# Optimization experiments

Measured on AMD Instinct MI355X. Metric: run time of the kernel, lower is better.

The kernel has to match this reference:

```python
import jax, jax.numpy as jnp
import numpy as np

GH = 256       # GRU hidden size
VOCAB = 1000
MAX_EP = 150
NPREV = NCURR = NNEXT = 64


def _gru_scan(emb, h0, wih, whh, bih, bhh):
    # torch nn.GRU single-layer math, scanned over the token axis
    H = h0.shape[0]
    def step(h, x_t):
        gi = wih @ x_t + bih            # [3H]
        gh = whh @ h + bhh              # [3H]
        r = jax.nn.sigmoid(gi[:H] + gh[:H])
        z = jax.nn.sigmoid(gi[H:2 * H] + gh[H:2 * H])
        n = jnp.tanh(gi[2 * H:] + r * gh[2 * H:])
        hn = (1.0 - z) * n + z * h
        return hn, hn
    _, hs = jax.lax.scan(step, h0, emb)
    return hs                            # [L, H]


def _conv(x, w, b, s):
    y = jax.lax.conv_general_dilated(x, w, (s, s), 'VALID',
                                     dimension_numbers=('NCHW', 'OIHW', 'NCHW'))
    return y + b[None, :, None, None]


def setup_inputs():
    key = jax.random.key(0)
    ks = jax.random.split(key, 48)
    f32 = jnp.float32
    def W(i, shape, s=0.05):
        return (jax.random.normal(ks[i], shape) * s).astype(f32)
    inp = dict(
        x=jax.random.normal(ks[0], (1, 3, 124, 124), f32),
        hx=jax.random.normal(ks[1], (1, 256), f32),
        cx=jax.random.normal(ks[2], (1, 256), f32),
        conv1_w=W(3, (128, 3, 8, 8)), conv1_b=jnp.zeros((128,), f32),
        conv2_w=W(4, (64, 128, 4, 4)), conv2_b=jnp.zeros((64,), f32),
        conv3_w=W(5, (64, 64, 4, 4)), conv3_b=jnp.zeros((64,), f32),
        emb_w=W(6, (VOCAB, 32), 1.0),
        gru_f_wih=W(7, (3 * GH, 32)), gru_f_whh=W(8, (3 * GH, GH)),
        gru_f_bih=jnp.zeros((3 * GH,), f32), gru_f_bhh=jnp.zeros((3 * GH,), f32),
        gru_b_wih=W(9, (3 * GH, 32)), gru_b_whh=W(10, (3 * GH, GH)),
        gru_b_bih=jnp.zeros((3 * GH,), f32), gru_b_bhh=jnp.zeros((3 * GH,), f32),
        time_emb_w=W(11, (MAX_EP + 1, 32), 1.0),
        temp_emb_w=W(12, (2, 32), 1.0),
        img_emb_w=W(13, (256, 64 * 6 * 6)), img_emb_b=jnp.zeros((256,), f32),
        attn_key_w=W(14, (256, 256 * 3)), attn_key_b=jnp.zeros((256,), f32),
        bilinear_A=W(15, (1, 256, 544)), bilinear_b=jnp.zeros((1,), f32),
        reduce_w=W(16, (128, 544)), reduce_b=jnp.zeros((128,), f32),
        gate_w=W(17, (64, 640)), gate_b=jnp.zeros((64,), f32),
        lin_w=W(18, (256, 64 * 6 * 6)), lin_b=jnp.zeros((256,), f32),
        lstm_wih=W(19, (1024, 256)), lstm_whh=W(20, (1024, 256)),
        lstm_bih=jnp.zeros((1024,), f32), lstm_bhh=jnp.zeros((1024,), f32),
        critic_w=W(21, (1, 288)), critic_b=jnp.zeros((1,), f32),
        actor_w=W(22, (4, 288)), actor_b=jnp.zeros((4,), f32),
        prev_inst=jax.random.randint(ks[23], (1, NPREV), 0, VOCAB),
        curr_inst=jax.random.randint(ks[24], (1, NCURR), 0, VOCAB),
        next_inst=jax.random.randint(ks[25], (1, NNEXT), 0, VOCAB),
        tx=jax.random.randint(ks[26], (1,), 0, MAX_EP + 1),
    )
    return inp


def reference(x, hx, cx, conv1_w, conv1_b, conv2_w, conv2_b, conv3_w, conv3_b,
              emb_w, gru_f_wih, gru_f_whh, gru_f_bih, gru_f_bhh,
              gru_b_wih, gru_b_whh, gru_b_bih, gru_b_bhh,
              time_emb_w, temp_emb_w, img_emb_w, img_emb_b,
              attn_key_w, attn_key_b, bilinear_A, bilinear_b,
              reduce_w, reduce_b, gate_w, gate_b, lin_w, lin_b,
              lstm_wih, lstm_whh, lstm_bih, lstm_bhh,
              critic_w, critic_b, actor_w, actor_b,
              prev_inst, curr_inst, next_inst, tx):
    np_, nc, nn_ = prev_inst.shape[1], curr_inst.shape[1], next_inst.shape[1]
    all_inst = jnp.concatenate([prev_inst, curr_inst, next_inst], axis=1)[0]  # [L]
    L = all_inst.shape[0]

    # CNN encoder
    h = jax.nn.relu(_conv(x, conv1_w, conv1_b, 4))
    h = jax.nn.relu(_conv(h, conv2_w, conv2_b, 2))
    x_img = jax.nn.relu(_conv(h, conv3_w, conv3_b, 2))       # [1,64,6,6]

    # token-looped GRUs -> single lax.scan each (note: original runs gru_b
    # over the SAME forward order then reverses the hidden list; replicated)
    emb = emb_w[all_inst]                                    # [L,32]
    h0 = jnp.zeros((GH,), emb.dtype)
    hs_f = _gru_scan(emb, h0, gru_f_wih, gru_f_whh, gru_f_bih, gru_f_bhh)
    hs_b = _gru_scan(emb, h0, gru_b_wih, gru_b_whh, gru_b_bih, gru_b_bhh)[::-1]
    curr_instr_rep = jnp.concatenate([hs_f[np_ + nc - 1], hs_b[np_]])[None]  # [1,512]
    ir_f = jnp.concatenate([hs_f[:np_], hs_f[L - nn_:]], axis=0)             # [M,256]
    ir_b = jnp.concatenate([hs_b[:np_], hs_b[L - nn_:]], axis=0)
    temp_tok = jnp.concatenate([jnp.zeros((np_,), jnp.int32), jnp.ones((nn_,), jnp.int32)])
    instr_rep = jnp.concatenate([ir_f, ir_b, temp_emb_w[temp_tok]], axis=1)  # [M,544]

    # bilinear attention over prev/next token states
    image_emb = x_img.reshape(1, -1) @ img_emb_w.T + img_emb_b               # [1,256]
    attn_key = jnp.concatenate([curr_instr_rep, image_emb], 1) @ attn_key_w.T + attn_key_b
    scores = jnp.einsum('k,okv,mv->mo', attn_key[0], bilinear_A, instr_rep) + bilinear_b  # [M,1]
    w = jax.nn.softmax(scores, axis=0)
    instr_sum = (instr_rep * w).sum(0, keepdims=True)                        # [1,544]

    # gating of image features
    gating = instr_sum @ reduce_w.T + reduce_b                               # [1,128]
    gate_key = jax.nn.sigmoid(jnp.concatenate([curr_instr_rep, gating], 1) @ gate_w.T + gate_b)  # [1,64]
    xg = (x_img * gate_key[:, :, None, None]).reshape(1, -1)
    z = jax.nn.relu(xg @ lin_w.T + lin_b)                                    # [1,256]

    # LSTMCell (torch gate order i,f,g,o)
    gates = z @ lstm_wih.T + lstm_bih + hx @ lstm_whh.T + lstm_bhh           # [1,1024]
    i, f, g, o = jnp.split(gates, 4, axis=1)
    cx2 = jax.nn.sigmoid(f) * cx + jax.nn.sigmoid(i) * jnp.tanh(g)
    hx2 = jax.nn.sigmoid(o) * jnp.tanh(cx2)

    feat = jnp.concatenate([hx2, time_emb_w[tx].reshape(-1, 32)], axis=1)    # [1,288]
    critic = feat @ critic_w.T + critic_b                                    # [1,1]
    actor = feat @ actor_w.T + actor_b                                       # [1,4]
    return critic, actor, hx2, cx2
```

## Files before the change

kernel.cpp:

```cpp
#include <hip/hip_runtime.h>
#include <hip/hip_bf16.h>

typedef int int4v __attribute__((ext_vector_type(4)));

__device__ __forceinline__ float bf2f(unsigned short u) {
    unsigned int v = ((unsigned int)u) << 16;
    return __builtin_bit_cast(float, v);
}
__device__ __forceinline__ float sigm(float x) { return 1.0f / (1.0f + expf(-x)); }
__device__ __forceinline__ float san(float v) {
    return (v == v && fabsf(v) < 1e20f) ? v : 12345.0f;
}
__device__ __forceinline__ void wrout(void* out, int i, float v, int f32out) {
    if (f32out) ((float*)out)[i] = v;
    else ((__hip_bfloat16*)out)[i] = __float2bfloat16(v);
}
__device__ __forceinline__ float fexp2(float x) {
#if __has_builtin(__builtin_amdgcn_exp2f)
    return __builtin_amdgcn_exp2f(x);
#else
    return exp2f(x);
#endif
}
__device__ __forceinline__ float frcp(float x) {
#if __has_builtin(__builtin_amdgcn_rcpf)
    return __builtin_amdgcn_rcpf(x);
#else
    return 1.0f / x;
#endif
}
__device__ __forceinline__ float fsigm(float x) {
    return frcp(1.0f + fexp2(x * -1.44269504f));
}
__device__ __forceinline__ float ftanh(float x) {
    float t = fexp2(x * 2.88539008f);
    return 1.0f - 2.0f * frcp(t + 1.0f);
}
__device__ __forceinline__ float wave_red(float acc) {
#pragma unroll
    for (int off = 32; off >= 1; off >>= 1) acc += __shfl_down(acc, off);
    return acc;
}
__device__ __forceinline__ int sel4(int4v v, int rg) {
    int a = (rg & 1) ? v.y : v.x;
    int b = (rg & 1) ? v.w : v.z;
    return (rg & 2) ? b : a;
}

struct CanonArgs {
    const void* ptr[40];
    int start[41];
    int size[40];
};

__global__ void k_flag1000(void* out) {
    if (threadIdx.x == 0) ((unsigned int*)out)[0] = 0x447A0000u;
}

__global__ void k_detect_tokens(const void* x, int nx,
                                const int* __restrict__ prev, const int* __restrict__ curr,
                                const int* __restrict__ nxt, const int* __restrict__ tx,
                                float* __restrict__ flags, int* __restrict__ toks) {
    __shared__ float sm[256];
    __shared__ int sInt64;
    int tid = threadIdx.x;
    const unsigned short* xs = (const unsigned short*)x;
    float mx = 0.0f;
    for (int i = tid; i < nx; i += 256) {
        float f = bf2f(xs[i]);
        float a = (f == f) ? fabsf(f) : 1e30f;
        mx = fmaxf(mx, a);
    }
    sm[tid] = mx;
    __syncthreads();
    for (int s = 128; s >= 1; s >>= 1) {
        if (tid < s) sm[tid] = fmaxf(sm[tid], sm[tid + s]);
        __syncthreads();
    }
    if (tid == 0) {
        flags[0] = (sm[0] > 100.0f) ? 1.0f : 0.0f;
        int anyOdd = 0;
        for (int k = 0; k < 32; ++k) anyOdd |= curr[2 * k + 1];
        int i64 = (anyOdd == 0) ? 1 : 0;
        flags[1] = (float)i64;
        sInt64 = i64;
    }
    __syncthreads();
    int stride = sInt64 ? 2 : 1;
    if (tid < 192) {
        const int* src = (tid < 64) ? prev : ((tid < 128) ? curr : nxt);
        int v = src[(tid & 63) * stride];
        toks[tid] = min(max(v, 0), 999);
    }
    if (tid == 0) toks[192] = min(max(tx[0], 0), 150);
}

__global__ void k_convert(CanonArgs a, const float* __restrict__ flags,
                          float* __restrict__ C) {
    int base = blockIdx.x << 10;
    int t = 0;
    while (t < 39 && base >= a.start[t + 1]) ++t;
    int local = base - a.start[t] + (threadIdx.x << 2);
    int sz = a.size[t];
    float4 v = make_float4(0.0f, 0.0f, 0.0f, 0.0f);
    int f32in = (flags[0] != 0.0f);
    if (local + 3 < sz) {
        if (f32in) {
            v = *(const float4*)((const float*)a.ptr[t] + local);
        } else {
            uint2 u = *(const uint2*)((const unsigned short*)a.ptr[t] + local);
            v.x = bf2f((unsigned short)(u.x & 0xffff));
            v.y = bf2f((unsigned short)(u.x >> 16));
            v.z = bf2f((unsigned short)(u.y & 0xffff));
            v.w = bf2f((unsigned short)(u.y >> 16));
        }
    } else if (local < sz) {
        float tmp[4] = {0.0f, 0.0f, 0.0f, 0.0f};
        for (int q = 0; q < 4 && local + q < sz; ++q) {
            if (f32in) tmp[q] = ((const float*)a.ptr[t])[local + q];
            else tmp[q] = bf2f(((const unsigned short*)a.ptr[t])[local + q]);
        }
        v = make_float4(tmp[0], tmp[1], tmp[2], tmp[3]);
    }
    *(float4*)(C + base + (threadIdx.x << 2)) = v;
}

__global__ void k_conv1(const float* __restrict__ x, const float* __restrict__ w,
                        const float* __restrict__ b, float* __restrict__ out) {
    int idx = blockIdx.x * 256 + threadIdx.x;
    int oc = idx / 900;
    int rem = idx - oc * 900;
    int oh = rem / 30;
    int ow = rem - oh * 30;
    float acc = b[oc];
    for (int ic = 0; ic < 3; ++ic) {
        int xb = ic * 15376 + (oh * 4) * 124 + ow * 4;
        int wb = oc * 192 + ic * 64;
#pragma unroll
        for (int kh = 0; kh < 8; ++kh) {
            const float2* xr = (const float2*)(x + xb + kh * 124);
            const float2* wr = (const float2*)(w + wb + kh * 8);
#pragma unroll
            for (int p = 0; p < 4; ++p) {
                float2 xv = xr[p];
                float2 wv = wr[p];
                acc += xv.x * wv.x + xv.y * wv.y;
            }
        }
    }
    out[idx] = fmaxf(acc, 0.0f);
}

__global__ void k_conv2(const float* __restrict__ in, const float* __restrict__ w,
                        const float* __restrict__ b, float* __restrict__ out) {
    int wid = (blockIdx.x * 256 + threadIdx.x) >> 6;
    int lane = threadIdx.x & 63;
    int oc = wid / 196;
    int rem = wid - oc * 196;
    int oh = rem / 14, ow = rem - oh * 14;
    float acc = 0.0f;
#pragma unroll 8
    for (int i = 0; i < 32; ++i) {
        int e = lane + (i << 6);
        int ic = e >> 4, k = e & 15, kh = k >> 2, kw = k & 3;
        acc += in[ic * 900 + (oh * 2 + kh) * 30 + ow * 2 + kw] * w[oc * 2048 + e];
    }
    acc = wave_red(acc);
    if (lane == 0) out[wid] = fmaxf(acc + b[oc], 0.0f);
}

__global__ void k_conv3(const float* __restrict__ in, const float* __restrict__ w,
                        const float* __restrict__ b, float* __restrict__ out) {
    int wid = (blockIdx.x * 256 + threadIdx.x) >> 6;
    int lane = threadIdx.x & 63;
    int oc = wid / 36;
    int rem = wid - oc * 36;
    int oh = rem / 6, ow = rem - oh * 6;
    float acc = 0.0f;
#pragma unroll
    for (int i = 0; i < 16; ++i) {
        int e = lane + (i << 6);
        int ic = e >> 4, k = e & 15, kh = k >> 2, kw = k & 3;
        acc += in[ic * 196 + (oh * 2 + kh) * 14 + ow * 2 + kw] * w[oc * 1024 + e];
    }
    acc = wave_red(acc);
    if (lane == 0) out[wid] = fmaxf(acc + b[oc], 0.0f);
}

__global__ void k_imgemb(const float* __restrict__ ximg, const float* __restrict__ w,
                         const float* __restrict__ b, float* __restrict__ out) {
    int j = blockIdx.x;
    int t = threadIdx.x;
    const float* wr = w + j * 2304;
    float acc = 0.0f;
    for (int k = t; k < 2304; k += 64) acc += wr[k] * ximg[k];
    acc = wave_red(acc);
    if (t == 0) out[j] = acc + b[j];
}

__global__ void k_gi(const int* __restrict__ toks, const float* __restrict__ emb,
                     const float* __restrict__ wih_f, const float* __restrict__ bih_f,
                     const float* __restrict__ bhh_f,
                     const float* __restrict__ wih_b, const float* __restrict__ bih_b,
                     const float* __restrict__ bhh_b,
                     float* __restrict__ gi) {
    int t = blockIdx.y;
    int gru = blockIdx.z;
    int j = blockIdx.x * 256 + threadIdx.x;
    __shared__ float e[32];
    int tok = toks[t];
    if (threadIdx.x < 32) e[threadIdx.x] = emb[tok * 32 + threadIdx.x];
    __syncthreads();
    const float* wih = gru ? wih_b : wih_f;
    const float* bih = gru ? bih_b : bih_f;
    const float* bhh = gru ? bhh_b : bhh_f;
    const float2* wr = (const float2*)(wih + j * 32);
    float acc = bih[j] + ((j < 512) ? bhh[j] : 0.0f);
#pragma unroll
    for (int k = 0; k < 16; ++k) {
        float2 wv = wr[k];
        acc += wv.x * e[2 * k] + wv.y * e[2 * k + 1];
    }
    gi[(gru * 192 + t) * 768 + j] = acc;
}

__global__ __launch_bounds__(512, 1) void k_gru(
    const float* __restrict__ whh_f, const float* __restrict__ bhh_f,
    const float* __restrict__ whh_b, const float* __restrict__ bhh_b,
    const float* __restrict__ gi, float* __restrict__ hs) {
    __shared__ unsigned int hq[2][64];
    __shared__ float sc[768];

    int gru = blockIdx.x;
    const float* whh = gru ? whh_b : whh_f;
    const float* bhh = gru ? bhh_b : bhh_f;
    const float* gib = gi + gru * 192 * 768;
    float* hso = hs + gru * 192 * 256;

    int t = threadIdx.x;
    int l = t & 63;
    int w = t >> 6;
    int lg = l >> 4;
    int lr = l & 15;
    int e_sel = (l >> 2) & 1;
    int rg = l & 3;
    int j = 32 * w + 16 * e_sel + 4 * lg + rg;

    int4v A[3][2][4];
#pragma unroll
    for (int s3 = 0; s3 < 3; ++s3) {
#pragma unroll
        for (int e = 0; e < 2; ++e) {
            int r = s3 * 256 + 32 * w + 16 * e + lr;
            const float* rowp = whh + r * 256;
            float4 tmp[16];
            float mx = 0.0f;
#pragma unroll
            for (int q = 0; q < 4; ++q) {
#pragma unroll
                for (int f = 0; f < 4; ++f) {
                    float4 v = *(const float4*)(rowp + 64 * q + 16 * lg + 4 * f);
                    tmp[q * 4 + f] = v;
                    mx = fmaxf(mx, fmaxf(fmaxf(fabsf(v.x), fabsf(v.y)),
                                         fmaxf(fabsf(v.z), fabsf(v.w))));
                }
            }
            mx = fmaxf(mx, __shfl_xor(mx, 16));
            mx = fmaxf(mx, __shfl_xor(mx, 32));
            float scale = 127.0f / fmaxf(mx, 1e-20f);
            if (lg == 0) sc[r] = mx * (1.0f / (127.0f * 127.0f));
#pragma unroll
            for (int q = 0; q < 4; ++q) {
                int dw[4];
#pragma unroll
                for (int f = 0; f < 4; ++f) {
                    float4 v = tmp[q * 4 + f];
                    int p0 = (int)rintf(v.x * scale) & 0xff;
                    int p1 = (int)rintf(v.y * scale) & 0xff;
                    int p2 = (int)rintf(v.z * scale) & 0xff;
                    int p3 = (int)rintf(v.w * scale);
                    dw[f] = p0 | (p1 << 8) | (p2 << 16) | (p3 << 24);
                }
                A[s3][e][q] = (int4v){dw[0], dw[1], dw[2], dw[3]};
            }
        }
    }
    if (t < 128) ((unsigned int*)hq)[t] = 0u;
    __syncthreads();

    float invR = sc[j];
    float invZ = sc[256 + j];
    float invN = sc[512 + j];
    float bhhn = bhh[512 + j];
    int wr8 = ((l & 8) == 0);

    float hprev = 0.0f;
    float cr0 = gib[j],       cz0 = gib[256 + j],  cn0 = gib[512 + j];
    float cr1 = gib[768 + j], cz1 = gib[1024 + j], cn1 = gib[1280 + j];

    int4v zero4 = (int4v){0, 0, 0, 0};

    auto step = [&](const unsigned int* hbuf, unsigned int* hnxt, int S,
                    float gr, float gz, float gn) {
        const char* hb = (const char*)hbuf;
        int4v B0 = *(const int4v*)(hb + 16 * lg);
        int4v B1 = *(const int4v*)(hb + 64 + 16 * lg);
        int4v B2 = *(const int4v*)(hb + 128 + 16 * lg);
        int4v B3 = *(const int4v*)(hb + 192 + 16 * lg);

        int4v C00, C01, C10, C11, C20, C21;
        asm volatile(
            "v_mfma_i32_16x16x64_i8 %0, %7,  %31, %6\n\t"
            "v_mfma_i32_16x16x64_i8 %1, %11, %31, %6\n\t"
            "v_mfma_i32_16x16x64_i8 %2, %15, %31, %6\n\t"
            "v_mfma_i32_16x16x64_i8 %3, %19, %31, %6\n\t"
            "v_mfma_i32_16x16x64_i8 %4, %23, %31, %6\n\t"
            "v_mfma_i32_16x16x64_i8 %5, %27, %31, %6\n\t"
            "v_mfma_i32_16x16x64_i8 %0, %8,  %32, %0\n\t"
            "v_mfma_i32_16x16x64_i8 %1, %12, %32, %1\n\t"
            "v_mfma_i32_16x16x64_i8 %2, %16, %32, %2\n\t"
            "v_mfma_i32_16x16x64_i8 %3, %20, %32, %3\n\t"
            "v_mfma_i32_16x16x64_i8 %4, %24, %32, %4\n\t"
            "v_mfma_i32_16x16x64_i8 %5, %28, %32, %5\n\t"
            "v_mfma_i32_16x16x64_i8 %0, %9,  %33, %0\n\t"
            "v_mfma_i32_16x16x64_i8 %1, %13, %33, %1\n\t"
            "v_mfma_i32_16x16x64_i8 %2, %17, %33, %2\n\t"
            "v_mfma_i32_16x16x64_i8 %3, %21, %33, %3\n\t"
            "v_mfma_i32_16x16x64_i8 %4, %25, %33, %4\n\t"
            "v_mfma_i32_16x16x64_i8 %5, %29, %33, %5\n\t"
            "v_mfma_i32_16x16x64_i8 %0, %10, %34, %0\n\t"
            "v_mfma_i32_16x16x64_i8 %1, %14, %34, %1\n\t"
            "v_mfma_i32_16x16x64_i8 %2, %18, %34, %2\n\t"
            "v_mfma_i32_16x16x64_i8 %3, %22, %34, %3\n\t"
            "v_mfma_i32_16x16x64_i8 %4, %26, %34, %4\n\t"
            "v_mfma_i32_16x16x64_i8 %5, %30, %34, %5\n\t"
            "s_nop 7\n\t"
            "s_nop 7"
            : "=&v"(C00), "=&v"(C01), "=&v"(C10),
              "=&v"(C11), "=&v"(C20), "=&v"(C21)
            : "v"(zero4),
              "v"(A[0][0][0]), "v"(A[0][0][1]), "v"(A[0][0][2]), "v"(A[0][0][3]),
              "v"(A[0][1][0]), "v"(A[0][1][1]), "v"(A[0][1][2]), "v"(A[0][1][3]),
              "v"(A[1][0][0]), "v"(A[1][0][1]), "v"(A[1][0][2]), "v"(A[1][0][3]),
              "v"(A[1][1][0]), "v"(A[1][1][1]), "v"(A[1][1][2]), "v"(A[1][1][3]),
              "v"(A[2][0][0]), "v"(A[2][0][1]), "v"(A[2][0][2]), "v"(A[2][0][3]),
              "v"(A[2][1][0]), "v"(A[2][1][1]), "v"(A[2][1][2]), "v"(A[2][1][3]),
              "v"(B0), "v"(B1), "v"(B2), "v"(B3));
        __builtin_amdgcn_sched_barrier(0);

        int ri = sel4(e_sel ? C01 : C00, rg);
        int zi = sel4(e_sel ? C11 : C10, rg);
        int ni = sel4(e_sel ? C21 : C20, rg);
        float ar = (float)ri * invR;
        float az = (float)zi * invZ;
        float an = (float)ni * invN;
        float r = fsigm(gr + ar);
        float z = fsigm(gz + az);
        float n = ftanh(gn + r * (an + bhhn));
        hprev = z * (hprev - n) + n;

        int qv = (int)rintf(hprev * 127.0f);
        if (wr8) {
            hso[S * 256 + j] = hprev;
            ((char*)hnxt)[j] = (char)qv;
        }
        asm volatile("s_waitcnt lgkmcnt(0)" ::: "memory");
        __builtin_amdgcn_s_barrier();
    };

    for (int i = 0; i < 96; ++i) {
        int s0 = 2 * i;
        float nr0 = 0.0f, nz0 = 0.0f, nn0 = 0.0f;
        if (s0 + 2 < 192) {
            const float* gp = gib + (s0 + 2) * 768 + j;
            nr0 = gp[0]; nz0 = gp[256]; nn0 = gp[512];
        }
        step(&hq[0][0], &hq[1][0], s0, cr0, cz0, cn0);

        int s1 = s0 + 1;
        float nr1 = 0.0f, nz1 = 0.0f, nn1 = 0.0f;
        if (s1 + 2 < 192) {
            const float* gp = gib + (s1 + 2) * 768 + j;
            nr1 = gp[0]; nz1 = gp[256]; nn1 = gp[512];
        }
        step(&hq[1][0], &hq[0][0], s1, cr1, cz1, cn1);

        cr0 = nr0; cz0 = nz0; cn0 = nn0;
        cr1 = nr1; cz1 = nz1; cn1 = nn1;
    }
}

__device__ __forceinline__ float ir_val(int m, int v, const float* hsf, const float* hsb,
                                        const float* temp_emb) {
    if (v < 256) { int r = (m < 64) ? m : 64 + m; return hsf[r * 256 + v]; }
    if (v < 512) { int r = (m < 64) ? 191 - m : 127 - m; return hsb[r * 256 + v - 256]; }
    return temp_emb[(m >= 64) * 32 + (v - 512)];
}

__global__ void k_attnkey(const float* __restrict__ hs, const float* __restrict__ imgemb,
                          const float* __restrict__ w, const float* __restrict__ b,
                          float* __restrict__ ak) {
    int j = blockIdx.x;
    int t = threadIdx.x;
    const float* hsf127 = hs + 127 * 256;
    const float* hsb127 = hs + 192 * 256 + 127 * 256;
    const float* wr = w + j * 768;
    float acc = 0.0f;
    for (int k = t; k < 768; k += 64) {
        float v = (k < 256) ? hsf127[k] : ((k < 512) ? hsb127[k - 256] : imgemb[k - 512]);
        acc += wr[k] * v;
    }
    acc = wave_red(acc);
    if (t == 0) ak[j] = acc + b[j];
}

__global__ void k_bilin(const float* __restrict__ A, const float* __restrict__ ak,
                        float* __restrict__ tmp) {
    int v = blockIdx.x;
    int t = threadIdx.x;
    float acc = 0.0f;
#pragma unroll
    for (int k = t; k < 256; k += 64) acc += A[k * 544 + v] * ak[k];
    acc = wave_red(acc);
    if (t == 0) tmp[v] = acc;
}

__global__ __launch_bounds__(1024) void k_attnmid(
    const float* __restrict__ hs, const float* __restrict__ temp_emb_w,
    const float* __restrict__ tmpv, const float* __restrict__ bb,
    const float* __restrict__ reduce_w, const float* __restrict__ reduce_b,
    const float* __restrict__ gate_w, const float* __restrict__ gate_b,
    float* __restrict__ gk) {
    const int tid = threadIdx.x;
    const float* hsf = hs;
    const float* hsb = hs + 192 * 256;
    __shared__ float stmp[544], ssc[128], ssum[544], sred[1024], sgating[128], scr[512];

    if (tid < 256) {
        scr[tid] = hsf[127 * 256 + tid];
        scr[256 + tid] = hsb[127 * 256 + tid];
    }
    if (tid < 544) stmp[tid] = tmpv[tid];
    __syncthreads();

    {
        int m = tid >> 3, q = tid & 7;
        float acc = 0.0f;
        for (int v = q * 68; v < q * 68 + 68; ++v) acc += stmp[v] * ir_val(m, v, hsf, hsb, temp_emb_w);
        sred[tid] = acc;
    }
    __syncthreads();
    if (tid < 128) {
        float acc = bb[0];
        for (int q = 0; q < 8; ++q) acc += sred[tid * 8 + q];
        ssc[tid] = acc;
        sred[tid] = acc;
    }
    __syncthreads();
#pragma unroll
    for (int s2 = 64; s2 >= 1; s2 >>= 1) {
        if (tid < s2) sred[tid] = fmaxf(sred[tid], sred[tid + s2]);
        __syncthreads();
    }
    float mx = sred[0];
    __syncthreads();
    if (tid < 128) {
        float e = expf(ssc[tid] - mx);
        ssc[tid] = e;
        sred[tid] = e;
    }
    __syncthreads();
#pragma unroll
    for (int s2 = 64; s2 >= 1; s2 >>= 1) {
        if (tid < s2) sred[tid] += sred[tid + s2];
        __syncthreads();
    }
    float inv = 1.0f / sred[0];
    __syncthreads();
    if (tid < 128) ssc[tid] *= inv;
    __syncthreads();

    if (tid < 544) {
        float acc = 0.0f;
        for (int m = 0; m < 128; ++m) acc += ssc[m] * ir_val(m, tid, hsf, hsb, temp_emb_w);
        ssum[tid] = acc;
    }
    __syncthreads();

    {
        int j = tid >> 3, q = tid & 7;
        const float2* wr = (const float2*)(reduce_w + j * 544 + q * 68);
        float acc = 0.0f;
        for (int k = 0; k < 34; ++k) {
            float2 wv = wr[k];
            acc += wv.x * ssum[q * 68 + 2 * k] + wv.y * ssum[q * 68 + 2 * k + 1];
        }
        sred[tid] = acc;
    }
    __syncthreads();
    if (tid < 128) {
        float acc = reduce_b[tid];
        for (int q = 0; q < 8; ++q) acc += sred[tid * 8 + q];
        sgating[tid] = acc;
    }
    __syncthreads();

    {
        int j = tid >> 4, q = tid & 15;
        const float2* wr = (const float2*)(gate_w + j * 640 + q * 40);
        float acc = 0.0f;
        for (int k = 0; k < 20; ++k) {
            float2 wv = wr[k];
            int v0 = q * 40 + 2 * k;
            float a0 = (v0 < 512) ? scr[v0] : sgating[v0 - 512];
            float a1 = (v0 + 1 < 512) ? scr[v0 + 1] : sgating[v0 + 1 - 512];
            acc += wv.x * a0 + wv.y * a1;
        }
        sred[tid] = acc;
    }
    __syncthreads();
    if (tid < 64) {
        float acc = gate_b[tid];
        for (int q = 0; q < 16; ++q) acc += sred[tid * 16 + q];
        gk[tid] = sigm(acc);
    }
}

__global__ void k_lin(const float* __restrict__ ximg, const float* __restrict__ gk,
                      const float* __restrict__ w, const float* __restrict__ b,
                      float* __restrict__ z) {
    int j = blockIdx.x;
    int t = threadIdx.x;
    __shared__ float sgk[64];
    if (t < 64) sgk[t] = gk[t];
    __syncthreads();
    const float* wr = w + j * 2304;
    float acc = 0.0f;
    for (int k = t; k < 2304; k += 64) acc += wr[k] * ximg[k] * sgk[k / 36];
    acc = wave_red(acc);
    if (t == 0) z[j] = fmaxf(acc + b[j], 0.0f);
}

__global__ void k_lstm(const float* __restrict__ z, const float* __restrict__ hx,
                       const float* __restrict__ wih, const float* __restrict__ whh,
                       const float* __restrict__ bih, const float* __restrict__ bhh,
                       float* __restrict__ sg) {
    int j = blockIdx.x;
    int t = threadIdx.x;
    const float* wi = wih + j * 256;
    const float* wh = whh + j * 256;
    float acc = 0.0f;
#pragma unroll
    for (int k = t; k < 256; k += 64) acc += wi[k] * z[k] + wh[k] * hx[k];
    acc = wave_red(acc);
    if (t == 0) sg[j] = acc + bih[j] + bhh[j];
}

__global__ __launch_bounds__(1024) void k_final(
    const float* __restrict__ sgg, const float* __restrict__ cx,
    const float* __restrict__ time_emb_w, const int* __restrict__ toks,
    const float* __restrict__ critic_w, const float* __restrict__ critic_b,
    const float* __restrict__ actor_w, const float* __restrict__ actor_b,
    const float* __restrict__ flags, void* __restrict__ out) {
    const int tid = threadIdx.x;
    __shared__ float sfeat[288], shx2[256], scx2[256], stmp[544], sred[1024];

    if (tid < 256) {
        float ii = sgg[tid], ff = sgg[256 + tid], gg = sgg[512 + tid], oo = sgg[768 + tid];
        float c2 = sigm(ff) * cx[tid] + sigm(ii) * tanhf(gg);
        float h2 = sigm(oo) * tanhf(c2);
        scx2[tid] = c2;
        shx2[tid] = h2;
        sfeat[tid] = h2;
    }
    if (tid < 32) sfeat[256 + tid] = time_emb_w[toks[192] * 32 + tid];
    __syncthreads();

    if (tid < 512) stmp[tid] = (tid < 288) ? critic_w[tid] * sfeat[tid] : 0.0f;
    {
        int a = tid >> 8, k = tid & 255;
        float pa = actor_w[a * 288 + k] * sfeat[k];
        if (k < 32) pa += actor_w[a * 288 + 256 + k] * sfeat[256 + k];
        sred[tid] = pa;
    }
    __syncthreads();
#pragma unroll
    for (int s2 = 256; s2 >= 1; s2 >>= 1) {
        if (tid < s2) stmp[tid] += stmp[tid + s2];
        int k = tid & 255;
        if (s2 <= 128 && k < s2) sred[tid] += sred[tid + s2];
        __syncthreads();
    }

    int f32out = (flags[0] != 0.0f) ? 1 : 0;
    if (tid == 0) wrout(out, 0, san(stmp[0] + critic_b[0]), f32out);
    if (tid < 4) wrout(out, 1 + tid, san(sred[tid * 256] + actor_b[tid]), f32out);
    if (tid < 256) {
        wrout(out, 5 + tid, san(shx2[tid]), f32out);
        wrout(out, 261 + tid, san(scx2[tid]), f32out);
    }
}

extern "C" void kernel_launch(void* const* d_in, const int* in_sizes, int n_in,
                              void* d_out, int out_size, void* d_ws, size_t ws_size,
                              hipStream_t stream) {
    if (n_in != 44) return;

    CanonArgs ca;
    int acc = 0;
    for (int i = 0; i < 40; ++i) {
        ca.ptr[i] = d_in[i];
        ca.start[i] = acc;
        ca.size[i] = in_sizes[i];
        acc += (in_sizes[i] + 1023) & ~1023;
    }
    ca.start[40] = acc;
    const int T = acc;

    float* ws     = (float*)d_ws;
    float* flags  = ws;
    int*   toks   = (int*)(ws + 64);
    float* imgemb = ws + 320;
    float* C      = ws + 640;
    float* gi     = C + T;
    float* hs     = gi + 294912;
    float* aux    = hs + 98304;
    float* ak     = aux;
    float* tmpv   = aux + 256;
    float* gk     = aux + 928;
    float* zv     = aux + 992;
    float* sg     = aux + 1248;
    float* h1     = gi;
    float* h2     = h1 + 115200;
    float* ximg   = h2 + 12544;

    size_t need = (size_t)(640 + T + 294912 + 98304 + 2272) * 4;
    if (ws_size < need) {
        k_flag1000<<<1, 64, 0, stream>>>(d_out);
        return;
    }

    const int* prev = (const int*)d_in[40];
    const int* curr = (const int*)d_in[41];
    const int* nxt  = (const int*)d_in[42];
    const int* tx   = (const int*)d_in[43];

    k_detect_tokens<<<1, 256, 0, stream>>>(d_in[0], in_sizes[0], prev, curr, nxt, tx,
                                           flags, toks);
    k_convert<<<T >> 10, 256, 0, stream>>>(ca, flags, C);

#define CP(i) (C + ca.start[i])
    k_gi<<<dim3(3, 192, 2), 256, 0, stream>>>(toks, CP(9),
                                              CP(10), CP(12), CP(13),
                                              CP(14), CP(16), CP(17), gi);
    k_gru<<<2, 512, 0, stream>>>(CP(11), CP(13), CP(15), CP(17), gi, hs);
    k_conv1<<<450, 256, 0, stream>>>(CP(0), CP(3), CP(4), h1);
    k_conv2<<<3136, 256, 0, stream>>>(h1, CP(5), CP(6), h2);
    k_conv3<<<576, 256, 0, stream>>>(h2, CP(7), CP(8), ximg);
    k_imgemb<<<256, 64, 0, stream>>>(ximg, CP(20), CP(21), imgemb);
    k_attnkey<<<256, 64, 0, stream>>>(hs, imgemb, CP(22), CP(23), ak);
    k_bilin<<<544, 64, 0, stream>>>(CP(24), ak, tmpv);
    k_attnmid<<<1, 1024, 0, stream>>>(hs, CP(19), tmpv, CP(25),
                                      CP(26), CP(27), CP(28), CP(29), gk);
    k_lin<<<256, 64, 0, stream>>>(ximg, gk, CP(30), CP(31), zv);
    k_lstm<<<1024, 64, 0, stream>>>(zv, CP(1), CP(32), CP(33), CP(34), CP(35), sg);
    k_final<<<1, 1024, 0, stream>>>(sg, CP(2), CP(18), toks,
                                    CP(36), CP(37), CP(38), CP(39), flags, d_out);
#undef CP
}
```

Before: 482.8 us.

## Overlap GRU recurrence with conv stack in one kernel and fuse tail kernels

Merges the two-block GRU scan and the conv1/conv2/conv3/image-embedding chain into one persistent kernel. Blocks 0-1 run the GRU while 128 other blocks run the convolutions, separated by a grid-wide atomic barrier, so the image path runs in the GRU's shadow. The attention, gating, linear, LSTM and output kernels are folded into a single 1024-thread tail kernel to remove launch overheads. The cost is a spin barrier that relies on all blocks being co-resident, and a single block doing the tail matvecs with less parallelism.

Result: slower. 736.9 us (+52.6%).

```diff
diff --git a/kernel.cpp b/kernel.cpp
--- a/kernel.cpp
+++ b/kernel.cpp
@@ -2,6 +2,8 @@
 #include <hip/hip_bf16.h>
 
 typedef int int4v __attribute__((ext_vector_type(4)));
+
+#define CBLK 128
 
 __device__ __forceinline__ float bf2f(unsigned short u) {
     unsigned int v = ((unsigned int)u) << 16;
@@ -45,6 +47,18 @@
     int a = (rg & 1) ? v.y : v.x;
     int b = (rg & 1) ? v.w : v.z;
     return (rg & 2) ? b : a;
+}
+
+__device__ __forceinline__ void gbar(unsigned int* bar, unsigned int target) {
+    __syncthreads();
+    if (threadIdx.x == 0) {
+        __threadfence();
+        atomicAdd(bar, 1u);
+        while (__hip_atomic_load(bar, __ATOMIC_RELAXED, __HIP_MEMORY_SCOPE_AGENT) < target)
+            __builtin_amdgcn_s_sleep(2);
+        __threadfence();
+    }
+    __syncthreads();
 }
 
 struct CanonArgs {
@@ -125,79 +139,6 @@
     *(float4*)(C + base + (threadIdx.x << 2)) = v;
 }
 
-__global__ void k_conv1(const float* __restrict__ x, const float* __restrict__ w,
-                        const float* __restrict__ b, float* __restrict__ out) {
-    int idx = blockIdx.x * 256 + threadIdx.x;
-    int oc = idx / 900;
-    int rem = idx - oc * 900;
-    int oh = rem / 30;
-    int ow = rem - oh * 30;
-    float acc = b[oc];
-    for (int ic = 0; ic < 3; ++ic) {
-        int xb = ic * 15376 + (oh * 4) * 124 + ow * 4;
-        int wb = oc * 192 + ic * 64;
-#pragma unroll
-        for (int kh = 0; kh < 8; ++kh) {
-            const float2* xr = (const float2*)(x + xb + kh * 124);
-            const float2* wr = (const float2*)(w + wb + kh * 8);
-#pragma unroll
-            for (int p = 0; p < 4; ++p) {
-                float2 xv = xr[p];
-                float2 wv = wr[p];
-                acc += xv.x * wv.x + xv.y * wv.y;
-            }
-        }
-    }
-    out[idx] = fmaxf(acc, 0.0f);
-}
-
-__global__ void k_conv2(const float* __restrict__ in, const float* __restrict__ w,
-                        const float* __restrict__ b, float* __restrict__ out) {
-    int wid = (blockIdx.x * 256 + threadIdx.x) >> 6;
-    int lane = threadIdx.x & 63;
-    int oc = wid / 196;
-    int rem = wid - oc * 196;
-    int oh = rem / 14, ow = rem - oh * 14;
-    float acc = 0.0f;
-#pragma unroll 8
-    for (int i = 0; i < 32; ++i) {
-        int e = lane + (i << 6);
-        int ic = e >> 4, k = e & 15, kh = k >> 2, kw = k & 3;
-        acc += in[ic * 900 + (oh * 2 + kh) * 30 + ow * 2 + kw] * w[oc * 2048 + e];
-    }
-    acc = wave_red(acc);
-    if (lane == 0) out[wid] = fmaxf(acc + b[oc], 0.0f);
-}
-
-__global__ void k_conv3(const float* __restrict__ in, const float* __restrict__ w,
-                        const float* __restrict__ b, float* __restrict__ out) {
-    int wid = (blockIdx.x * 256 + threadIdx.x) >> 6;
-    int lane = threadIdx.x & 63;
-    int oc = wid / 36;
-    int rem = wid - oc * 36;
-    int oh = rem / 6, ow = rem - oh * 6;
-    float acc = 0.0f;
-#pragma unroll
-    for (int i = 0; i < 16; ++i) {
-        int e = lane + (i << 6);
-        int ic = e >> 4, k = e & 15, kh = k >> 2, kw = k & 3;
-        acc += in[ic * 196 + (oh * 2 + kh) * 14 + ow * 2 + kw] * w[oc * 1024 + e];
-    }
-    acc = wave_red(acc);
-    if (lane == 0) out[wid] = fmaxf(acc + b[oc], 0.0f);
-}
-
-__global__ void k_imgemb(const float* __restrict__ ximg, const float* __restrict__ w,
-                         const float* __restrict__ b, float* __restrict__ out) {
-    int j = blockIdx.x;
-    int t = threadIdx.x;
-    const float* wr = w + j * 2304;
-    float acc = 0.0f;
-    for (int k = t; k < 2304; k += 64) acc += wr[k] * ximg[k];
-    acc = wave_red(acc);
-    if (t == 0) out[j] = acc + b[j];
-}
-
 __global__ void k_gi(const int* __restrict__ toks, const float* __restrict__ emb,
                      const float* __restrict__ wih_f, const float* __restrict__ bih_f,
                      const float* __restrict__ bhh_f,
@@ -224,169 +165,247 @@
     gi[(gru * 192 + t) * 768 + j] = acc;
 }
 
-__global__ __launch_bounds__(512, 1) void k_gru(
-    const float* __restrict__ whh_f, const float* __restrict__ bhh_f,
-    const float* __restrict__ whh_b, const float* __restrict__ bhh_b,
-    const float* __restrict__ gi, float* __restrict__ hs) {
+struct BigArgs {
+    const float *whh_f, *bhh_f, *whh_b, *bhh_b, *gi;
+    float* hs;
+    const float *x, *c1w, *c1b, *c2w, *c2b, *c3w, *c3b, *iew, *ieb;
+    float *h1, *xh2, *ximg, *imgemb;
+    unsigned int* bars;
+};
+
+__global__ __launch_bounds__(512, 1) void k_big(BigArgs a) {
     __shared__ unsigned int hq[2][64];
     __shared__ float sc[768];
-
-    int gru = blockIdx.x;
-    const float* whh = gru ? whh_b : whh_f;
-    const float* bhh = gru ? bhh_b : bhh_f;
-    const float* gib = gi + gru * 192 * 768;
-    float* hso = hs + gru * 192 * 256;
-
-    int t = threadIdx.x;
-    int l = t & 63;
-    int w = t >> 6;
-    int lg = l >> 4;
-    int lr = l & 15;
-    int e_sel = (l >> 2) & 1;
-    int rg = l & 3;
-    int j = 32 * w + 16 * e_sel + 4 * lg + rg;
-
-    int4v A[3][2][4];
-#pragma unroll
-    for (int s3 = 0; s3 < 3; ++s3) {
-#pragma unroll
-        for (int e = 0; e < 2; ++e) {
-            int r = s3 * 256 + 32 * w + 16 * e + lr;
-            const float* rowp = whh + r * 256;
-            float4 tmp[16];
-            float mx = 0.0f;
-#pragma unroll
-            for (int q = 0; q < 4; ++q) {
-#pragma unroll
-                for (int f = 0; f < 4; ++f) {
-                    float4 v = *(const float4*)(rowp + 64 * q + 16 * lg + 4 * f);
-                    tmp[q * 4 + f] = v;
-                    mx = fmaxf(mx, fmaxf(fmaxf(fabsf(v.x), fabsf(v.y)),
-                                         fmaxf(fabsf(v.z), fabsf(v.w))));
+    const int B = blockIdx.x;
+    const int tid = threadIdx.x;
+
+    if (B < 2) {
+        const float* whh = B ? a.whh_b : a.whh_f;
+        const float* bhh = B ? a.bhh_b : a.bhh_f;
+        const float* gib = a.gi + B * 192 * 768;
+        float* hso = a.hs + B * 192 * 256;
+
+        int t = tid;
+        int l = t & 63;
+        int w = t >> 6;
+        int lg = l >> 4;
+        int lr = l & 15;
+        int e_sel = (l >> 2) & 1;
+        int rg = l & 3;
+        int j = 32 * w + 16 * e_sel + 4 * lg + rg;
+
+        int4v A[3][2][4];
+#pragma unroll
+        for (int s3 = 0; s3 < 3; ++s3) {
+#pragma unroll
+            for (int e = 0; e < 2; ++e) {
+                int r = s3 * 256 + 32 * w + 16 * e + lr;
+                const float* rowp = whh + r * 256;
+                float4 tmp[16];
+                float mx = 0.0f;
+#pragma unroll
+                for (int q = 0; q < 4; ++q) {
+#pragma unroll
+                    for (int f = 0; f < 4; ++f) {
+                        float4 v = *(const float4*)(rowp + 64 * q + 16 * lg + 4 * f);
+                        tmp[q * 4 + f] = v;
+                        mx = fmaxf(mx, fmaxf(fmaxf(fabsf(v.x), fabsf(v.y)),
+                                             fmaxf(fabsf(v.z), fabsf(v.w))));
+                    }
+                }
+                mx = fmaxf(mx, __shfl_xor(mx, 16));
+                mx = fmaxf(mx, __shfl_xor(mx, 32));
+                float scale = 127.0f / fmaxf(mx, 1e-20f);
+                if (lg == 0) sc[r] = mx * (1.0f / (127.0f * 127.0f));
+#pragma unroll
+                for (int q = 0; q < 4; ++q) {
+                    int dw[4];
+#pragma unroll
+                    for (int f = 0; f < 4; ++f) {
+                        float4 v = tmp[q * 4 + f];
+                        int p0 = (int)rintf(v.x * scale) & 0xff;
+                        int p1 = (int)rintf(v.y * scale) & 0xff;
+                        int p2 = (int)rintf(v.z * scale) & 0xff;
+                        int p3 = (int)rintf(v.w * scale);
+                        dw[f] = p0 | (p1 << 8) | (p2 << 16) | (p3 << 24);
+                    }
+                    A[s3][e][q] = (int4v){dw[0], dw[1], dw[2], dw[3]};
                 }
             }
-            mx = fmaxf(mx, __shfl_xor(mx, 16));
-            mx = fmaxf(mx, __shfl_xor(mx, 32));
-            float scale = 127.0f / fmaxf(mx, 1e-20f);
-            if (lg == 0) sc[r] = mx * (1.0f / (127.0f * 127.0f));
-#pragma unroll
-            for (int q = 0; q < 4; ++q) {
-                int dw[4];
-#pragma unroll
-                for (int f = 0; f < 4; ++f) {
-                    float4 v = tmp[q * 4 + f];
-                    int p0 = (int)rintf(v.x * scale) & 0xff;
-                    int p1 = (int)rintf(v.y * scale) & 0xff;
-                    int p2 = (int)rintf(v.z * scale) & 0xff;
-                    int p3 = (int)rintf(v.w * scale);
-                    dw[f] = p0 | (p1 << 8) | (p2 << 16) | (p3 << 24);
+        }
+        if (t < 128) ((unsigned int*)hq)[t] = 0u;
+        __syncthreads();
+
+        float invR = sc[j];
+        float invZ = sc[256 + j];
+        float invN = sc[512 + j];
+        float bhhn = bhh[512 + j];
+        int wr8 = ((l & 8) == 0);
+
+        float hprev = 0.0f;
+        float cr0 = gib[j],       cz0 = gib[256 + j],  cn0 = gib[512 + j];
+        float cr1 = gib[768 + j], cz1 = gib[1024 + j], cn1 = gib[1280 + j];
+
+        int4v zero4 = (int4v){0, 0, 0, 0};
+
+        auto step = [&](const unsigned int* hbuf, unsigned int* hnxt, int S,
+                        float gr, float gz, float gn) {
+            const char* hb = (const char*)hbuf;
+            int4v B0 = *(const int4v*)(hb + 16 * lg);
+            int4v B1 = *(const int4v*)(hb + 64 + 16 * lg);
+            int4v B2 = *(const int4v*)(hb + 128 + 16 * lg);
+            int4v B3 = *(const int4v*)(hb + 192 + 16 * lg);
+
+            int4v C00, C01, C10, C11, C20, C21;
+            asm volatile(
+                "v_mfma_i32_16x16x64_i8 %0, %7,  %31, %6\n\t"
+                "v_mfma_i32_16x16x64_i8 %1, %11, %31, %6\n\t"
+                "v_mfma_i32_16x16x64_i8 %2, %15, %31, %6\n\t"
+                "v_mfma_i32_16x16x64_i8 %3, %19, %31, %6\n\t"
+                "v_mfma_i32_16x16x64_i8 %4, %23, %31, %6\n\t"
+                "v_mfma_i32_16x16x64_i8 %5, %27, %31, %6\n\t"
+                "v_mfma_i32_16x16x64_i8 %0, %8,  %32, %0\n\t"
+                "v_mfma_i32_16x16x64_i8 %1, %12, %32, %1\n\t"
+                "v_mfma_i32_16x16x64_i8 %2, %16, %32, %2\n\t"
+                "v_mfma_i32_16x16x64_i8 %3, %20, %32, %3\n\t"
+                "v_mfma_i32_16x16x64_i8 %4, %24, %32, %4\n\t"
+                "v_mfma_i32_16x16x64_i8 %5, %28, %32, %5\n\t"
+                "v_mfma_i32_16x16x64_i8 %0, %9,  %33, %0\n\t"
+                "v_mfma_i32_16x16x64_i8 %1, %13, %33, %1\n\t"
+                "v_mfma_i32_16x16x64_i8 %2, %17, %33, %2\n\t"
+                "v_mfma_i32_16x16x64_i8 %3, %21, %33, %3\n\t"
+                "v_mfma_i32_16x16x64_i8 %4, %25, %33, %4\n\t"
+                "v_mfma_i32_16x16x64_i8 %5, %29, %33, %5\n\t"
+                "v_mfma_i32_16x16x64_i8 %0, %10, %34, %0\n\t"
+                "v_mfma_i32_16x16x64_i8 %1, %14, %34, %1\n\t"
+                "v_mfma_i32_16x16x64_i8 %2, %18, %34, %2\n\t"
+                "v_mfma_i32_16x16x64_i8 %3, %22, %34, %3\n\t"
+                "v_mfma_i32_16x16x64_i8 %4, %26, %34, %4\n\t"
+                "v_mfma_i32_16x16x64_i8 %5, %30, %34, %5\n\t"
+                "s_nop 7\n\t"
+                "s_nop 7"
+                : "=&v"(C00), "=&v"(C01), "=&v"(C10),
+                  "=&v"(C11), "=&v"(C20), "=&v"(C21)
+                : "v"(zero4),
+                  "v"(A[0][0][0]), "v"(A[0][0][1]), "v"(A[0][0][2]), "v"(A[0][0][3]),
+                  "v"(A[0][1][0]), "v"(A[0][1][1]), "v"(A[0][1][2]), "v"(A[0][1][3]),
+                  "v"(A[1][0][0]), "v"(A[1][0][1]), "v"(A[1][0][2]), "v"(A[1][0][3]),
+                  "v"(A[1][1][0]), "v"(A[1][1][1]), "v"(A[1][1][2]), "v"(A[1][1][3]),
+                  "v"(A[2][0][0]), "v"(A[2][0][1]), "v"(A[2][0][2]), "v"(A[2][0][3]),
+                  "v"(A[2][1][0]), "v"(A[2][1][1]), "v"(A[2][1][2]), "v"(A[2][1][3]),
+                  "v"(B0), "v"(B1), "v"(B2), "v"(B3));
+            __builtin_amdgcn_sched_barrier(0);
+
+            int ri = sel4(e_sel ? C01 : C00, rg);
+            int zi = sel4(e_sel ? C11 : C10, rg);
+            int ni = sel4(e_sel ? C21 : C20, rg);
+            float ar = (float)ri * invR;
+            float az = (float)zi * invZ;
+            float an = (float)ni * invN;
+            float r = fsigm(gr + ar);
+            float z = fsigm(gz + az);
+            float n = ftanh(gn + r * (an + bhhn));
+            hprev = z * (hprev - n) + n;
+
+            int qv = (int)rintf(hprev * 127.0f);
+            if (wr8) {
+                hso[S * 256 + j] = hprev;
+                ((char*)hnxt)[j] = (char)qv;
+            }
+            asm volatile("s_waitcnt lgkmcnt(0)" ::: "memory");
+            __builtin_amdgcn_s_barrier();
+        };
+
+        for (int i = 0; i < 96; ++i) {
+            int s0 = 2 * i;
+            float nr0 = 0.0f, nz0 = 0.0f, nn0 = 0.0f;
+            if (s0 + 2 < 192) {
+                const float* gp = gib + (s0 + 2) * 768 + j;
+                nr0 = gp[0]; nz0 = gp[256]; nn0 = gp[512];
+            }
+            step(&hq[0][0], &hq[1][0], s0, cr0, cz0, cn0);
+
+            int s1 = s0 + 1;
+            float nr1 = 0.0f, nz1 = 0.0f, nn1 = 0.0f;
+            if (s1 + 2 < 192) {
+                const float* gp = gib + (s1 + 2) * 768 + j;
+                nr1 = gp[0]; nz1 = gp[256]; nn1 = gp[512];
+            }
+            step(&hq[1][0], &hq[0][0], s1, cr1, cz1, cn1);
+
+            cr0 = nr0; cz0 = nz0; cn0 = nn0;
+            cr1 = nr1; cz1 = nz1; cn1 = nn1;
+        }
+        return;
+    }
+
+    const int cb = B - 2;
+    const int lane = tid & 63;
+    const int cw = cb * 8 + (tid >> 6);
+
+    for (int idx = cb * 512 + tid; idx < 115200; idx += CBLK * 512) {
+        int oc = idx / 900;
+        int rem = idx - oc * 900;
+        int oh = rem / 30;
+        int ow = rem - oh * 30;
+        float acc = a.c1b[oc];
+        for (int ic = 0; ic < 3; ++ic) {
+            int xb = ic * 15376 + (oh * 4) * 124 + ow * 4;
+            int wb = oc * 192 + ic * 64;
+#pragma unroll
+            for (int kh = 0; kh < 8; ++kh) {
+                const float2* xr = (const float2*)(a.x + xb + kh * 124);
+                const float2* wr = (const float2*)(a.c1w + wb + kh * 8);
+#pragma unroll
+                for (int p = 0; p < 4; ++p) {
+                    float2 xv = xr[p];
+                    float2 wv = wr[p];
+                    acc += xv.x * wv.x + xv.y * wv.y;
                 }
-                A[s3][e][q] = (int4v){dw[0], dw[1], dw[2], dw[3]};
             }
         }
-    }
-    if (t < 128) ((unsigned int*)hq)[t] = 0u;
-    __syncthreads();
-
-    float invR = sc[j];
-    float invZ = sc[256 + j];
-    float invN = sc[512 + j];
-    float bhhn = bhh[512 + j];
-    int wr8 = ((l & 8) == 0);
-
-    float hprev = 0.0f;
-    float cr0 = gib[j],       cz0 = gib[256 + j],  cn0 = gib[512 + j];
-    float cr1 = gib[768 + j], cz1 = gib[1024 + j], cn1 = gib[1280 + j];
-
-    int4v zero4 = (int4v){0, 0, 0, 0};
-
-    auto step = [&](const unsigned int* hbuf, unsigned int* hnxt, int S,
-                    float gr, float gz, float gn) {
-        const char* hb = (const char*)hbuf;
-        int4v B0 = *(const int4v*)(hb + 16 * lg);
-        int4v B1 = *(const int4v*)(hb + 64 + 16 * lg);
-        int4v B2 = *(const int4v*)(hb + 128 + 16 * lg);
-        int4v B3 = *(const int4v*)(hb + 192 + 16 * lg);
-
-        int4v C00, C01, C10, C11, C20, C21;
-        asm volatile(
-            "v_mfma_i32_16x16x64_i8 %0, %7,  %31, %6\n\t"
-            "v_mfma_i32_16x16x64_i8 %1, %11, %31, %6\n\t"
-            "v_mfma_i32_16x16x64_i8 %2, %15, %31, %6\n\t"
-            "v_mfma_i32_16x16x64_i8 %3, %19, %31, %6\n\t"
-            "v_mfma_i32_16x16x64_i8 %4, %23, %31, %6\n\t"
-            "v_mfma_i32_16x16x64_i8 %5, %27, %31, %6\n\t"
-            "v_mfma_i32_16x16x64_i8 %0, %8,  %32, %0\n\t"
-            "v_mfma_i32_16x16x64_i8 %1, %12, %32, %1\n\t"
-            "v_mfma_i32_16x16x64_i8 %2, %16, %32, %2\n\t"
-            "v_mfma_i32_16x16x64_i8 %3, %20, %32, %3\n\t"
-            "v_mfma_i32_16x16x64_i8 %4, %24, %32, %4\n\t"
-            "v_mfma_i32_16x16x64_i8 %5, %28, %32, %5\n\t"
-            "v_mfma_i32_16x16x64_i8 %0, %9,  %33, %0\n\t"
-            "v_mfma_i32_16x16x64_i8 %1, %13, %33, %1\n\t"
-            "v_mfma_i32_16x16x64_i8 %2, %17, %33, %2\n\t"
-            "v_mfma_i32_16x16x64_i8 %3, %21, %33, %3\n\t"
-            "v_mfma_i32_16x16x64_i8 %4, %25, %33, %4\n\t"
-            "v_mfma_i32_16x16x64_i8 %5, %29, %33, %5\n\t"
-            "v_mfma_i32_16x16x64_i8 %0, %10, %34, %0\n\t"
-            "v_mfma_i32_16x16x64_i8 %1, %14, %34, %1\n\t"
-            "v_mfma_i32_16x16x64_i8 %2, %18, %34, %2\n\t"
-            "v_mfma_i32_16x16x64_i8 %3, %22, %34, %3\n\t"
-            "v_mfma_i32_16x16x64_i8 %4, %26, %34, %4\n\t"
-            "v_mfma_i32_16x16x64_i8 %5, %30, %34, %5\n\t"
-            "s_nop 7\n\t"
-            "s_nop 7"
-            : "=&v"(C00), "=&v"(C01), "=&v"(C10),
-              "=&v"(C11), "=&v"(C20), "=&v"(C21)
-            : "v"(zero4),
-              "v"(A[0][0][0]), "v"(A[0][0][1]), "v"(A[0][0][2]), "v"(A[0][0][3]),
-              "v"(A[0][1][0]), "v"(A[0][1][1]), "v"(A[0][1][2]), "v"(A[0][1][3]),
-              "v"(A[1][0][0]), "v"(A[1][0][1]), "v"(A[1][0][2]), "v"(A[1][0][3]),
-              "v"(A[1][1][0]), "v"(A[1][1][1]), "v"(A[1][1][2]), "v"(A[1][1][3]),
-              "v"(A[2][0][0]), "v"(A[2][0][1]), "v"(A[2][0][2]), "v"(A[2][0][3]),
-              "v"(A[2][1][0]), "v"(A[2][1][1]), "v"(A[2][1][2]), "v"(A[2][1][3]),
-              "v"(B0), "v"(B1), "v"(B2), "v"(B3));
-        __builtin_amdgcn_sched_barrier(0);
-
-        int ri = sel4(e_sel ? C01 : C00, rg);
-        int zi = sel4(e_sel ? C11 : C10, rg);
-        int ni = sel4(e_sel ? C21 : C20, rg);
-        float ar = (float)ri * invR;
-        float az = (float)zi * invZ;
-        float an = (float)ni * invN;
-        float r = fsigm(gr + ar);
-        float z = fsigm(gz + az);
-        float n = ftanh(gn + r * (an + bhhn));
-        hprev = z * (hprev - n) + n;
-
-        int qv = (int)rintf(hprev * 127.0f);
-        if (wr8) {
-            hso[S * 256 + j] = hprev;
-            ((char*)hnxt)[j] = (char)qv;
-        }
-        asm volatile("s_waitcnt lgkmcnt(0)" ::: "memory");
-        __builtin_amdgcn_s_barrier();
-    };
-
-    for (int i = 0; i < 96; ++i) {
-        int s0 = 2 * i;
-        float nr0 = 0.0f, nz0 = 0.0f, nn0 = 0.0f;
-        if (s0 + 2 < 192) {
-            const float* gp = gib + (s0 + 2) * 768 + j;
-            nr0 = gp[0]; nz0 = gp[256]; nn0 = gp[512];
-        }
-        step(&hq[0][0], &hq[1][0], s0, cr0, cz0, cn0);
-
-        int s1 = s0 + 1;
-        float nr1 = 0.0f, nz1 = 0.0f, nn1 = 0.0f;
-        if (s1 + 2 < 192) {
-            const float* gp = gib + (s1 + 2) * 768 + j;
-            nr1 = gp[0]; nz1 = gp[256]; nn1 = gp[512];
-        }
-        step(&hq[1][0], &hq[0][0], s1, cr1, cz1, cn1);
-
-        cr0 = nr0; cz0 = nz0; cn0 = nn0;
-        cr1 = nr1; cz1 = nz1; cn1 = nn1;
+        a.h1[idx] = fmaxf(acc, 0.0f);
+    }
+    gbar(a.bars + 0, CBLK);
+
+    for (int wid = cw; wid < 12544; wid += CBLK * 8) {
+        int oc = wid / 196;
+        int rem = wid - oc * 196;
+        int oh = rem / 14, ow = rem - oh * 14;
+        float acc = 0.0f;
+#pragma unroll 8
+        for (int i = 0; i < 32; ++i) {
+            int e = lane + (i << 6);
+            int ic = e >> 4, k = e & 15, kh = k >> 2, kw = k & 3;
+            acc += a.h1[ic * 900 + (oh * 2 + kh) * 30 + ow * 2 + kw] * a.c2w[oc * 2048 + e];
+        }
+        acc = wave_red(acc);
+        if (lane == 0) a.xh2[wid] = fmaxf(acc + a.c2b[oc], 0.0f);
+    }
+    gbar(a.bars + 1, CBLK);
+
+    for (int wid = cw; wid < 2304; wid += CBLK * 8) {
+        int oc = wid / 36;
+        int rem = wid - oc * 36;
+        int oh = rem / 6, ow = rem - oh * 6;
+        float acc = 0.0f;
+#pragma unroll
+        for (int i = 0; i < 16; ++i) {
+            int e = lane + (i << 6);
+            int ic = e >> 4, k = e & 15, kh = k >> 2, kw = k & 3;
+            acc += a.xh2[ic * 196 + (oh * 2 + kh) * 14 + ow * 2 + kw] * a.c3w[oc * 1024 + e];
+        }
+        acc = wave_red(acc);
+        if (lane == 0) a.ximg[wid] = fmaxf(acc + a.c3b[oc], 0.0f);
+    }
+    gbar(a.bars + 2, CBLK);
+
+    if (cw < 256) {
+        const float* wr = a.iew + cw * 2304;
+        float acc = 0.0f;
+        for (int k = lane; k < 2304; k += 64) acc += wr[k] * a.ximg[k];
+        acc = wave_red(acc);
+        if (lane == 0) a.imgemb[cw] = acc + a.ieb[cw];
     }
 }
 
@@ -397,61 +416,60 @@
     return temp_emb[(m >= 64) * 32 + (v - 512)];
 }
 
-__global__ void k_attnkey(const float* __restrict__ hs, const float* __restrict__ imgemb,
-                          const float* __restrict__ w, const float* __restrict__ b,
-                          float* __restrict__ ak) {
-    int j = blockIdx.x;
-    int t = threadIdx.x;
-    const float* hsf127 = hs + 127 * 256;
-    const float* hsb127 = hs + 192 * 256 + 127 * 256;
-    const float* wr = w + j * 768;
-    float acc = 0.0f;
-    for (int k = t; k < 768; k += 64) {
-        float v = (k < 256) ? hsf127[k] : ((k < 512) ? hsb127[k - 256] : imgemb[k - 512]);
-        acc += wr[k] * v;
-    }
-    acc = wave_red(acc);
-    if (t == 0) ak[j] = acc + b[j];
-}
-
-__global__ void k_bilin(const float* __restrict__ A, const float* __restrict__ ak,
-                        float* __restrict__ tmp) {
-    int v = blockIdx.x;
-    int t = threadIdx.x;
-    float acc = 0.0f;
-#pragma unroll
-    for (int k = t; k < 256; k += 64) acc += A[k * 544 + v] * ak[k];
-    acc = wave_red(acc);
-    if (t == 0) tmp[v] = acc;
-}
-
-__global__ __launch_bounds__(1024) void k_attnmid(
-    const float* __restrict__ hs, const float* __restrict__ temp_emb_w,
-    const float* __restrict__ tmpv, const float* __restrict__ bb,
-    const float* __restrict__ reduce_w, const float* __restrict__ reduce_b,
-    const float* __restrict__ gate_w, const float* __restrict__ gate_b,
-    float* __restrict__ gk) {
+struct TailArgs {
+    const float *hs, *imgemb, *ximg;
+    const float *akw, *akb, *bA, *bb, *temp;
+    const float *rw, *rb, *gw, *gb;
+    const float *lw, *lb;
+    const float *wih, *whh, *bih, *bhh, *hx, *cx, *te;
+    const float *crw, *crb, *acw, *acb, *flags;
+    const int* toks;
+    void* out;
+};
+
+__global__ __launch_bounds__(1024) void k_tail(TailArgs a) {
+    __shared__ float key[768], akl[256], stmp[544], ssc[128], ssum[544],
+        sred[1024], sgating[128], gkl[64], zvl[256], sgl[1024],
+        sfeat[320], sh2[256], sc2[256];
     const int tid = threadIdx.x;
-    const float* hsf = hs;
-    const float* hsb = hs + 192 * 256;
-    __shared__ float stmp[544], ssc[128], ssum[544], sred[1024], sgating[128], scr[512];
+    const int lane = tid & 63;
+    const int w = tid >> 6;
+    const float* hsf = a.hs;
+    const float* hsb = a.hs + 192 * 256;
 
     if (tid < 256) {
-        scr[tid] = hsf[127 * 256 + tid];
-        scr[256 + tid] = hsb[127 * 256 + tid];
-    }
-    if (tid < 544) stmp[tid] = tmpv[tid];
+        key[tid] = hsf[127 * 256 + tid];
+        key[256 + tid] = hsb[127 * 256 + tid];
+        key[512 + tid] = a.imgemb[tid];
+    }
+    __syncthreads();
+
+    for (int r = w; r < 256; r += 16) {
+        const float* wr = a.akw + r * 768;
+        float acc = 0.0f;
+        for (int k = lane; k < 768; k += 64) acc += wr[k] * key[k];
+        acc = wave_red(acc);
+        if (lane == 0) akl[r] = acc + a.akb[r];
+    }
+    __syncthreads();
+
+    if (tid < 544) {
+        float acc = 0.0f;
+        for (int k = 0; k < 256; ++k) acc += a.bA[k * 544 + tid] * akl[k];
+        stmp[tid] = acc;
+    }
     __syncthreads();
 
     {
         int m = tid >> 3, q = tid & 7;
         float acc = 0.0f;
-        for (int v = q * 68; v < q * 68 + 68; ++v) acc += stmp[v] * ir_val(m, v, hsf, hsb, temp_emb_w);
+        for (int v = q * 68; v < q * 68 + 68; ++v)
+            acc += stmp[v] * ir_val(m, v, hsf, hsb, a.temp);
         sred[tid] = acc;
     }
     __syncthreads();
     if (tid < 128) {
-        float acc = bb[0];
+        float acc = a.bb[0];
         for (int q = 0; q < 8; ++q) acc += sred[tid * 8 + q];
         ssc[tid] = acc;
         sred[tid] = acc;
@@ -482,14 +500,14 @@
 
     if (tid < 544) {
         float acc = 0.0f;
-        for (int m = 0; m < 128; ++m) acc += ssc[m] * ir_val(m, tid, hsf, hsb, temp_emb_w);
+        for (int m = 0; m < 128; ++m) acc += ssc[m] * ir_val(m, tid, hsf, hsb, a.temp);
         ssum[tid] = acc;
     }
     __syncthreads();
 
     {
         int j = tid >> 3, q = tid & 7;
-        const float2* wr = (const float2*)(reduce_w + j * 544 + q * 68);
+        const float2* wr = (const float2*)(a.rw + j * 544 + q * 68);
         float acc = 0.0f;
         for (int k = 0; k < 34; ++k) {
             float2 wv = wr[k];
@@ -499,7 +517,7 @@
     }
     __syncthreads();
     if (tid < 128) {
-        float acc = reduce_b[tid];
+        float acc = a.rb[tid];
         for (int q = 0; q < 8; ++q) acc += sred[tid * 8 + q];
         sgating[tid] = acc;
     }
@@ -507,80 +525,61 @@
 
     {
         int j = tid >> 4, q = tid & 15;
-        const float2* wr = (const float2*)(gate_w + j * 640 + q * 40);
+        const float2* wr = (const float2*)(a.gw + j * 640 + q * 40);
         float acc = 0.0f;
         for (int k = 0; k < 20; ++k) {
             float2 wv = wr[k];
             int v0 = q * 40 + 2 * k;
-            float a0 = (v0 < 512) ? scr[v0] : sgating[v0 - 512];
-            float a1 = (v0 + 1 < 512) ? scr[v0 + 1] : sgating[v0 + 1 - 512];
+            float a0 = (v0 < 512) ? key[v0] : sgating[v0 - 512];
+            float a1 = (v0 + 1 < 512) ? key[v0 + 1] : sgating[v0 + 1 - 512];
             acc += wv.x * a0 + wv.y * a1;
         }
         sred[tid] = acc;
     }
     __syncthreads();
     if (tid < 64) {
-        float acc = gate_b[tid];
+        float acc = a.gb[tid];
         for (int q = 0; q < 16; ++q) acc += sred[tid * 16 + q];
-        gk[tid] = sigm(acc);
-    }
-}
-
-__global__ void k_lin(const float* __restrict__ ximg, const float* __restrict__ gk,
-                      const float* __restrict__ w, const float* __restrict__ b,
-                      float* __restrict__ z) {
-    int j = blockIdx.x;
-    int t = threadIdx.x;
-    __shared__ float sgk[64];
-    if (t < 64) sgk[t] = gk[t];
-    __syncthreads();
-    const float* wr = w + j * 2304;
-    float acc = 0.0f;
-    for (int k = t; k < 2304; k += 64) acc += wr[k] * ximg[k] * sgk[k / 36];
-    acc = wave_red(acc);
-    if (t == 0) z[j] = fmaxf(acc + b[j], 0.0f);
-}
-
-__global__ void k_lstm(const float* __restrict__ z, const float* __restrict__ hx,
-                       const float* __restrict__ wih, const float* __restrict__ whh,
-                       const float* __restrict__ bih, const float* __restrict__ bhh,
-                       float* __restrict__ sg) {
-    int j = blockIdx.x;
-    int t = threadIdx.x;
-    const float* wi = wih + j * 256;
-    const float* wh = whh + j * 256;
-    float acc = 0.0f;
-#pragma unroll
-    for (int k = t; k < 256; k += 64) acc += wi[k] * z[k] + wh[k] * hx[k];
-    acc = wave_red(acc);
-    if (t == 0) sg[j] = acc + bih[j] + bhh[j];
-}
-
-__global__ __launch_bounds__(1024) void k_final(
-    const float* __restrict__ sgg, const float* __restrict__ cx,
-    const float* __restrict__ time_emb_w, const int* __restrict__ toks,
-    const float* __restrict__ critic_w, const float* __restrict__ critic_b,
-    const float* __restrict__ actor_w, const float* __restrict__ actor_b,
-    const float* __restrict__ flags, void* __restrict__ out) {
-    const int tid = threadIdx.x;
-    __shared__ float sfeat[288], shx2[256], scx2[256], stmp[544], sred[1024];
+        gkl[tid] = sigm(acc);
+    }
+    __syncthreads();
+
+    for (int r = w; r < 256; r += 16) {
+        const float* wr = a.lw + r * 2304;
+        float acc = 0.0f;
+        for (int k = lane; k < 2304; k += 64) acc += wr[k] * a.ximg[k] * gkl[k / 36];
+        acc = wave_red(acc);
+        if (lane == 0) zvl[r] = fmaxf(acc + a.lb[r], 0.0f);
+    }
+    __syncthreads();
+
+    for (int r = w; r < 1024; r += 16) {
+        const float* wi = a.wih + r * 256;
+        const float* wh = a.whh + r * 256;
+        float acc = 0.0f;
+#pragma unroll
+        for (int k = lane; k < 256; k += 64) acc += wi[k] * zvl[k] + wh[k] * a.hx[k];
+        acc = wave_red(acc);
+        if (lane == 0) sgl[r] = acc + a.bih[r] + a.bhh[r];
+    }
+    __syncthreads();
 
     if (tid < 256) {
-        float ii = sgg[tid], ff = sgg[256 + tid], gg = sgg[512 + tid], oo = sgg[768 + tid];
-        float c2 = sigm(ff) * cx[tid] + sigm(ii) * tanhf(gg);
+        float ii = sgl[tid], ff = sgl[256 + tid], gg = sgl[512 + tid], oo = sgl[768 + tid];
+        float c2 = sigm(ff) * a.cx[tid] + sigm(ii) * tanhf(gg);
         float h2 = sigm(oo) * tanhf(c2);
-        scx2[tid] = c2;
-        shx2[tid] = h2;
+        sc2[tid] = c2;
+        sh2[tid] = h2;
         sfeat[tid] = h2;
     }
-    if (tid < 32) sfeat[256 + tid] = time_emb_w[toks[192] * 32 + tid];
-    __syncthreads();
-
-    if (tid < 512) stmp[tid] = (tid < 288) ? critic_w[tid] * sfeat[tid] : 0.0f;
+    if (tid < 32) sfeat[256 + tid] = a.te[a.toks[192] * 32 + tid];
+    __syncthreads();
+
+    if (tid < 512) stmp[tid] = (tid < 288) ? a.crw[tid] * sfeat[tid] : 0.0f;
     {
-        int a = tid >> 8, k = tid & 255;
-        float pa = actor_w[a * 288 + k] * sfeat[k];
-        if (k < 32) pa += actor_w[a * 288 + 256 + k] * sfeat[256 + k];
+        int aa = tid >> 8, k = tid & 255;
+        float pa = a.acw[aa * 288 + k] * sfeat[k];
+        if (k < 32) pa += a.acw[aa * 288 + 256 + k] * sfeat[256 + k];
         sred[tid] = pa;
     }
     __syncthreads();
@@ -592,12 +591,12 @@
         __syncthreads();
     }
 
-    int f32out = (flags[0] != 0.0f) ? 1 : 0;
-    if (tid == 0) wrout(out, 0, san(stmp[0] + critic_b[0]), f32out);
-    if (tid < 4) wrout(out, 1 + tid, san(sred[tid * 256] + actor_b[tid]), f32out);
+    int f32out = (a.flags[0] != 0.0f) ? 1 : 0;
+    if (tid == 0) wrout(a.out, 0, san(stmp[0] + a.crb[0]), f32out);
+    if (tid < 4) wrout(a.out, 1 + tid, san(sred[tid * 256] + a.acb[tid]), f32out);
     if (tid < 256) {
-        wrout(out, 5 + tid, san(shx2[tid]), f32out);
-        wrout(out, 261 + tid, san(scx2[tid]), f32out);
+        wrout(a.out, 5 + tid, san(sh2[tid]), f32out);
+        wrout(a.out, 261 + tid, san(sc2[tid]), f32out);
     }
 }
 
@@ -619,22 +618,17 @@
 
     float* ws     = (float*)d_ws;
     float* flags  = ws;
+    unsigned int* bars = (unsigned int*)(ws + 32);
     int*   toks   = (int*)(ws + 64);
     float* imgemb = ws + 320;
     float* C      = ws + 640;
     float* gi     = C + T;
     float* hs     = gi + 294912;
-    float* aux    = hs + 98304;
-    float* ak     = aux;
-    float* tmpv   = aux + 256;
-    float* gk     = aux + 928;
-    float* zv     = aux + 992;
-    float* sg     = aux + 1248;
-    float* h1     = gi;
-    float* h2     = h1 + 115200;
-    float* ximg   = h2 + 12544;
-
-    size_t need = (size_t)(640 + T + 294912 + 98304 + 2272) * 4;
+    float* h1     = hs + 98304;
+    float* xh2    = h1 + 115200;
+    float* ximg   = xh2 + 12544;
+
+    size_t need = (size_t)(640 + T + 294912 + 98304 + 115200 + 12544 + 2304) * 4;
     if (ws_size < need) {
         k_flag1000<<<1, 64, 0, stream>>>(d_out);
         return;
@@ -645,26 +639,33 @@
     const int* nxt  = (const int*)d_in[42];
     const int* tx   = (const int*)d_in[43];
 
+#define CP(i) (C + ca.start[i])
+    hipMemsetAsync((char*)d_ws + 128, 0, 64, stream);
     k_detect_tokens<<<1, 256, 0, stream>>>(d_in[0], in_sizes[0], prev, curr, nxt, tx,
                                            flags, toks);
     k_convert<<<T >> 10, 256, 0, stream>>>(ca, flags, C);
-
-#define CP(i) (C + ca.start[i])
     k_gi<<<dim3(3, 192, 2), 256, 0, stream>>>(toks, CP(9),
                                               CP(10), CP(12), CP(13),
                                               CP(14), CP(16), CP(17), gi);
-    k_gru<<<2, 512, 0, stream>>>(CP(11), CP(13), CP(15), CP(17), gi, hs);
-    k_conv1<<<450, 256, 0, stream>>>(CP(0), CP(3), CP(4), h1);
-    k_conv2<<<3136, 256, 0, stream>>>(h1, CP(5), CP(6), h2);
-    k_conv3<<<576, 256, 0, stream>>>(h2, CP(7), CP(8), ximg);
-    k_imgemb<<<256, 64, 0, stream>>>(ximg, CP(20), CP(21), imgemb);
-    k_attnkey<<<256, 64, 0, stream>>>(hs, imgemb, CP(22), CP(23), ak);
-    k_bilin<<<544, 64, 0, stream>>>(CP(24), ak, tmpv);
-    k_attnmid<<<1, 1024, 0, stream>>>(hs, CP(19), tmpv, CP(25),
-                                      CP(26), CP(27), CP(28), CP(29), gk);
-    k_lin<<<256, 64, 0, stream>>>(ximg, gk, CP(30), CP(31), zv);
-    k_lstm<<<1024, 64, 0, stream>>>(zv, CP(1), CP(32), CP(33), CP(34), CP(35), sg);
-    k_final<<<1, 1024, 0, stream>>>(sg, CP(2), CP(18), toks,
-                                    CP(36), CP(37), CP(38), CP(39), flags, d_out);
+    BigArgs ba;
+    ba.whh_f = CP(11); ba.bhh_f = CP(13); ba.whh_b = CP(15); ba.bhh_b = CP(17);
+    ba.gi = gi; ba.hs = hs;
+    ba.x = CP(0); ba.c1w = CP(3); ba.c1b = CP(4);
+    ba.c2w = CP(5); ba.c2b = CP(6); ba.c3w = CP(7); ba.c3b = CP(8);
+    ba.iew = CP(20); ba.ieb = CP(21);
+    ba.h1 = h1; ba.xh2 = xh2; ba.ximg = ximg; ba.imgemb = imgemb;
+    ba.bars = bars;
+    k_big<<<2 + CBLK, 512, 0, stream>>>(ba);
+
+    TailArgs ta;
+    ta.hs = hs; ta.imgemb = imgemb; ta.ximg = ximg;
+    ta.akw = CP(22); ta.akb = CP(23); ta.bA = CP(24); ta.bb = CP(25); ta.temp = CP(19);
+    ta.rw = CP(26); ta.rb = CP(27); ta.gw = CP(28); ta.gb = CP(29);
+    ta.lw = CP(30); ta.lb = CP(31);
+    ta.wih = CP(32); ta.whh = CP(33); ta.bih = CP(34); ta.bhh = CP(35);
+    ta.hx = CP(1); ta.cx = CP(2); ta.te = CP(18);
+    ta.crw = CP(36); ta.crb = CP(37); ta.acw = CP(38); ta.acb = CP(39);
+    ta.flags = flags; ta.toks = toks; ta.out = d_out;
+    k_tail<<<1, 1024, 0, stream>>>(ta);
 #undef CP
 }
```
